# Performance work log

Measured on AMD Instinct MI355X. Metric: run time of the kernel, lower is better.

The kernel has to match this reference:

```python
import jax, jax.numpy as jnp
import numpy as np

H = 256  # hidden size; gates are 4H=1024 in PyTorch order i,f,g,o


def _lstm_layer(xs, W_ih, W_hh, b):
    """xs: (T, B, in) time-major. Returns (ys (T,B,H), (h_T, c_T))."""
    B = xs.shape[1]
    h0 = jnp.zeros((B, H), xs.dtype)
    c0 = jnp.zeros((B, H), xs.dtype)

    def step(carry, x_t):
        h, c = carry
        g = x_t @ W_ih.T + h @ W_hh.T + b  # (B, 4H)
        i, f, gg, o = jnp.split(g, 4, axis=-1)
        c = jax.nn.sigmoid(f) * c + jax.nn.sigmoid(i) * jnp.tanh(gg)
        h = jax.nn.sigmoid(o) * jnp.tanh(c)
        return (h, c), h

    (hT, cT), ys = jax.lax.scan(step, (h0, c0), xs)
    return ys, (hT, cT)


def setup_inputs() -> dict:
    key = jax.random.key(0)
    ks = jax.random.split(key, 9)
    B, T, D = 16, 8192, 7
    s = 0.05  # keep activations in a sane range
    return {
        "x": jax.random.normal(ks[0], (B, T, D), jnp.float32),
        "W_ih0": jax.random.normal(ks[1], (4 * H, D), jnp.float32) * s,
        "W_hh0": jax.random.normal(ks[2], (4 * H, H), jnp.float32) * s,
        "b0": jax.random.normal(ks[3], (4 * H,), jnp.float32) * s,
        "W_ih1": jax.random.normal(ks[4], (4 * H, H), jnp.float32) * s,
        "W_hh1": jax.random.normal(ks[5], (4 * H, H), jnp.float32) * s,
        "b1": jax.random.normal(ks[6], (4 * H,), jnp.float32) * s,
        "W_head": jax.random.normal(ks[7], (D, H), jnp.float32) * s,
        "b_head": jax.random.normal(ks[8], (D,), jnp.float32) * s,
    }


def reference(x, W_ih0, W_hh0, b0, W_ih1, W_hh1, b1, W_head, b_head):
    xs = jnp.transpose(x, (1, 0, 2))            # (T, B, D) time-major
    y0, (h0, c0) = _lstm_layer(xs, W_ih0, W_hh0, b0)
    y1, (h1, c1) = _lstm_layer(y0, W_ih1, W_hh1, b1)
    out = y1 @ W_head.T + b_head                # (T, B, out_dim)
    out = jnp.transpose(out, (1, 0, 2))         # (B, T, out_dim)
    h_n = jnp.stack([h0, h1])                   # (layers, B, H)
    c_n = jnp.stack([c0, c1])
    return (out, h_n, c_n)
```

## Files before the change

### kernel.cpp

```cpp
#include <hip/hip_runtime.h>
#include <hip/hip_bf16.h>

#define TT 8192
#define BB 16
#define HH 256
#define GG 8
#define NKS0 9
#define NKS1 16
#define ROW0 320
#define ROW1 512

typedef unsigned short u16;
typedef unsigned int   u32;
typedef __attribute__((ext_vector_type(4))) float f32x4;
typedef __attribute__((ext_vector_type(8))) short bf16x8;

union U16X8 { uint4 u; bf16x8 s; };

static const size_t OFF_SLOT = 0;
static const size_t OFF_H0   = 1024;
static const size_t OFF_H1   = 33792;
static const size_t OFF_A0   = 50176;
static const size_t OFF_A1   = 640000;
static const size_t OFF_Y1   = 1688576;

__device__ __forceinline__ float blo(u32 u){ return __uint_as_float(u << 16); }
__device__ __forceinline__ float bhi(u32 u){ return __uint_as_float(u & 0xffff0000u); }
__device__ __forceinline__ float sigf(float x){ return 1.0f/(1.0f + __expf(-x)); }
__device__ __forceinline__ float tanhf_(float x){ return 1.0f - 2.0f/(__expf(2.0f*x) + 1.0f); }
__device__ __forceinline__ u16 f2bf(float v){
  union { __hip_bfloat16 b; u16 s; } u; u.b = __float2bfloat16(v); return u.s;
}

__global__ __launch_bounds__(256) void pack_frags(
    const float* __restrict__ Wih0, const float* __restrict__ Whh0,
    const float* __restrict__ Wih1, const float* __restrict__ Whh1,
    u16* __restrict__ a0, u16* __restrict__ a1) {
  int idx = blockIdx.x*256 + threadIdx.x;
  const int N0 = GG*4*2*NKS0*512;
  const int N1 = GG*4*2*NKS1*512;
  if (idx < N0) {
    int i = idx;
    int ii = i & 511; int lane = ii >> 3; int e = ii & 7;
    int f = i >> 9; int ks = f % NKS0; f /= NKS0;
    int rt = f & 1; f >>= 1; int wq = f & 3; int g = f >> 2;
    int row = wq*256 + g*32 + rt*16 + (lane & 15);
    int k = ks*32 + (lane >> 4)*8 + e;
    float v = 0.0f;
    if (k < 7)                   v = Wih0[row*7 + k];
    else if (k >= 32 && k < 288) v = Whh0[row*256 + (k - 32)];
    a0[i] = f2bf(v);
  } else if (idx < N0 + N1) {
    int i = idx - N0;
    int ii = i & 511; int lane = ii >> 3; int e = ii & 7;
    int f = i >> 9; int ks = f & 15; f >>= 4;
    int rt = f & 1; f >>= 1; int wq = f & 3; int g = f >> 2;
    int row = wq*256 + g*32 + rt*16 + (lane & 15);
    int k = ks*32 + (lane >> 4)*8 + e;
    float v = (k < 256) ? Wih1[row*256 + k] : Whh1[row*256 + (k - 256)];
    a1[i] = f2bf(v);
  }
}

__device__ __forceinline__ void gang_wait(u32* slots_, int i, int tid, int l, int* budget) {
  if (i > 0) {
    if (tid < 64) {
      bool done = false;
      while (!done) {
        u32 v = 0xFFFFFFFFu;
        if (l < 16)
          v = __hip_atomic_load(&slots_[l*16], __ATOMIC_RELAXED, __HIP_MEMORY_SCOPE_AGENT);
        done = (bool)__all((int)(v >= (u32)i));
        if (!done) { __builtin_amdgcn_s_sleep(1); if (--(*budget) <= 0) done = true; }
      }
      (void)__hip_atomic_load(&slots_[0], __ATOMIC_ACQUIRE, __HIP_MEMORY_SCOPE_AGENT);
    }
    __syncthreads();
  }
}

__device__ __forceinline__ void gang_arrive(u32* slots_, int gb, int i, int tid) {
  asm volatile("s_waitcnt vmcnt(0)" ::: "memory");
  __syncthreads();
  if (tid == 0)
    __hip_atomic_store(&slots_[gb*16], (u32)(i + 1),
                       __ATOMIC_RELAXED, __HIP_MEMORY_SCOPE_AGENT);
}

__global__ __launch_bounds__(256, 1) void gangs(
    const float* __restrict__ x,
    const u16* __restrict__ a0, const u16* __restrict__ a1,
    const float* __restrict__ b0, const float* __restrict__ b1,
    u32* __restrict__ h0c, u32* __restrict__ h1c,
    u32* __restrict__ slots_, u32* __restrict__ y1ws,
    float* __restrict__ dout) {
  const int gb = blockIdx.x, tid = threadIdx.x;
  const int l = tid & 63, wq = tid >> 6;
  const int bb_ = l & 15, cq = l >> 4;
  const int pb = tid >> 4, pu = tid & 15;
  const int sb = tid >> 4, kg = tid & 15;
  __shared__ __align__(16) u16 hlds[16*ROW1];
  __shared__ float pre[4][32][17];
  uint4* lds4 = (uint4*)hlds;
  int budget = 3000000;
  float cst[2] = {0.f, 0.f}, hl[2] = {0.f, 0.f};

  if (gb < GG) {
    const int g = gb;
    uint4 A[2][NKS0];
    #pragma unroll
    for (int rt = 0; rt < 2; ++rt)
      #pragma unroll
      for (int ks = 0; ks < NKS0; ++ks)
        A[rt][ks] = ((const uint4*)a0)[ (((g*4 + wq)*2 + rt)*NKS0 + ks)*64 + l ];
    float bias4[2][4];
    #pragma unroll
    for (int rt = 0; rt < 2; ++rt)
      #pragma unroll
      for (int i = 0; i < 4; ++i)
        bias4[rt][i] = b0[wq*256 + g*32 + rt*16 + cq*4 + i];
    const int xb = tid >> 3, xj = tid & 7;
    for (int z = tid; z < 16*ROW0/2; z += 256) ((u32*)hlds)[z] = 0;
    __syncthreads();

    for (int i = 0; i < TT + 2; ++i) {
      const int t = i;
      const bool act = (t < TT);
      float xv = 0.0f;
      if (act && tid < 128 && xj < 7)
        xv = x[(size_t)xb*(TT*7) + (size_t)t*7 + xj];

      gang_wait(slots_, i, tid, l, &budget);

      if (act) {
        {
          const uint4* hb = (const uint4*)(h0c + ((t + 3) & 3)*2048 + sb*128 + kg*8);
          uint4 h0v = hb[0], h1v = hb[1];
          lds4[sb*40 + ((4 + 2*kg + 0) ^ (sb & 7))] = h0v;
          lds4[sb*40 + ((4 + 2*kg + 1) ^ (sb & 7))] = h1v;
        }
        if (tid < 128 && xj < 7)
          hlds[xb*ROW0 + ((xb & 7)*8) + xj] = f2bf(xv);
        __syncthreads();

        f32x4 acc[2];
        #pragma unroll
        for (int rt = 0; rt < 2; ++rt)
          acc[rt] = (f32x4){bias4[rt][0], bias4[rt][1], bias4[rt][2], bias4[rt][3]};
        #pragma unroll
        for (int ks = 0; ks < NKS0; ++ks) {
          U16X8 bfr; bfr.u = lds4[bb_*40 + ((ks*4 + cq) ^ (bb_ & 7))];
          U16X8 afr0; afr0.u = A[0][ks];
          U16X8 afr1; afr1.u = A[1][ks];
          acc[0] = __builtin_amdgcn_mfma_f32_16x16x32_bf16(afr0.s, bfr.s, acc[0], 0, 0, 0);
          acc[1] = __builtin_amdgcn_mfma_f32_16x16x32_bf16(afr1.s, bfr.s, acc[1], 0, 0, 0);
        }
        #pragma unroll
        for (int rt = 0; rt < 2; ++rt)
          #pragma unroll
          for (int ii = 0; ii < 4; ++ii)
            pre[wq][rt*16 + cq*4 + ii][bb_] = acc[rt][ii];
        __syncthreads();

        u32 packed;
        {
          #pragma unroll
          for (int e = 0; e < 2; ++e) {
            int u = 2*pu + e;
            float pi = pre[0][u][pb], pf = pre[1][u][pb],
                  pg = pre[2][u][pb], po = pre[3][u][pb];
            cst[e] = sigf(pf)*cst[e] + sigf(pi)*tanhf_(pg);
            hl[e]  = sigf(po)*tanhf_(cst[e]);
          }
          packed = (u32)f2bf(hl[0]) | ((u32)f2bf(hl[1]) << 16);
        }
        __hip_atomic_store(&h0c[(t & 3)*2048 + pb*128 + g*16 + pu], packed,
                           __ATOMIC_RELAXED, __HIP_MEMORY_SCOPE_AGENT);
      }
      gang_arrive(slots_, gb, i, tid);
    }
    #pragma unroll
    for (int e = 0; e < 2; ++e) {
      dout[917504 + pb*256 + g*32 + 2*pu + e] = hl[e];
      dout[925696 + pb*256 + g*32 + 2*pu + e] = cst[e];
    }
  } else {
    const int g = gb - GG;
    uint4 A[2][NKS1];
    #pragma unroll
    for (int rt = 0; rt < 2; ++rt)
      #pragma unroll
      for (int ks = 0; ks < NKS1; ++ks)
        A[rt][ks] = ((const uint4*)a1)[ (((g*4 + wq)*2 + rt)*NKS1 + ks)*64 + l ];
    float bias4[2][4];
    #pragma unroll
    for (int rt = 0; rt < 2; ++rt)
      #pragma unroll
      for (int i = 0; i < 4; ++i)
        bias4[rt][i] = b1[wq*256 + g*32 + rt*16 + cq*4 + i];
    __syncthreads();

    for (int i = 0; i < TT + 2; ++i) {
      const int t1 = i - 2;
      const bool act = (t1 >= 0);
      uint4 py[4];
      if (act && kg < 8) {
        const uint4* yb = (const uint4*)(h0c + (t1 & 3)*2048 + sb*128 + kg*16);
        #pragma unroll
        for (int m = 0; m < 4; ++m) py[m] = yb[m];
      }

      gang_wait(slots_, i, tid, l, &budget);

      if (act) {
        if (kg < 8) {
          #pragma unroll
          for (int m = 0; m < 4; ++m)
            lds4[sb*64 + ((4*kg + m) ^ (sb & 7))] = py[m];
        } else {
          const uint4* hb = (const uint4*)(h1c + (t1 & 1)*2048 + sb*128 + (kg - 8)*16);
          #pragma unroll
          for (int m = 0; m < 4; ++m)
            lds4[sb*64 + ((4*kg + m) ^ (sb & 7))] = hb[m];
        }
        __syncthreads();

        f32x4 acc[2];
        #pragma unroll
        for (int rt = 0; rt < 2; ++rt)
          acc[rt] = (f32x4){bias4[rt][0], bias4[rt][1], bias4[rt][2], bias4[rt][3]};
        #pragma unroll
        for (int ks = 0; ks < NKS1; ++ks) {
          U16X8 bfr; bfr.u = lds4[bb_*64 + ((ks*4 + cq) ^ (bb_ & 7))];
          U16X8 afr0; afr0.u = A[0][ks];
          U16X8 afr1; afr1.u = A[1][ks];
          acc[0] = __builtin_amdgcn_mfma_f32_16x16x32_bf16(afr0.s, bfr.s, acc[0], 0, 0, 0);
          acc[1] = __builtin_amdgcn_mfma_f32_16x16x32_bf16(afr1.s, bfr.s, acc[1], 0, 0, 0);
        }
        #pragma unroll
        for (int rt = 0; rt < 2; ++rt)
          #pragma unroll
          for (int ii = 0; ii < 4; ++ii)
            pre[wq][rt*16 + cq*4 + ii][bb_] = acc[rt][ii];
        __syncthreads();

        u32 packed;
        {
          #pragma unroll
          for (int e = 0; e < 2; ++e) {
            int u = 2*pu + e;
            float pi = pre[0][u][pb], pf = pre[1][u][pb],
                  pg = pre[2][u][pb], po = pre[3][u][pb];
            cst[e] = sigf(pf)*cst[e] + sigf(pi)*tanhf_(pg);
            hl[e]  = sigf(po)*tanhf_(cst[e]);
          }
          packed = (u32)f2bf(hl[0]) | ((u32)f2bf(hl[1]) << 16);
        }
        __hip_atomic_store(&h1c[((t1 + 1) & 1)*2048 + pb*128 + g*16 + pu], packed,
                           __ATOMIC_RELAXED, __HIP_MEMORY_SCOPE_AGENT);
        y1ws[(size_t)t1*2048 + pb*128 + g*16 + pu] = packed;
      }
      gang_arrive(slots_, gb, i, tid);
    }
    #pragma unroll
    for (int e = 0; e < 2; ++e) {
      dout[917504 + 4096 + pb*256 + g*32 + 2*pu + e] = hl[e];
      dout[925696 + 4096 + pb*256 + g*32 + 2*pu + e] = cst[e];
    }
  }
}

__global__ __launch_bounds__(256) void head_kernel(
    const u16* __restrict__ y1, const float* __restrict__ Wh,
    const float* __restrict__ bh, float* __restrict__ out) {
  __shared__ float wt[256][8];
  const int tid = threadIdx.x;
  for (int idx = tid; idx < 2048; idx += 256) {
    int j = idx >> 3, o = idx & 7;
    wt[j][o] = (o < 7) ? Wh[o*256 + j] : 0.0f;
  }
  __syncthreads();
  const int gidx = blockIdx.x*256 + tid;
  const int t = gidx >> 4, b = gidx & 15;
  const uint4* row = (const uint4*)(y1 + (size_t)t*4096 + b*256);
  float4 a03 = {0,0,0,0}, a47 = {0,0,0,0};
  #pragma unroll 4
  for (int jj = 0; jj < 32; ++jj) {
    uint4 v = row[jj];
    u32 ws_[4] = {v.x, v.y, v.z, v.w};
    #pragma unroll
    for (int m = 0; m < 4; ++m) {
      int j = jj*8 + 2*m;
      float h0 = blo(ws_[m]), h1 = bhi(ws_[m]);
      float4 w00 = *(const float4*)&wt[j][0],   w01 = *(const float4*)&wt[j][4];
      float4 w10 = *(const float4*)&wt[j+1][0], w11 = *(const float4*)&wt[j+1][4];
      a03.x += h0*w00.x; a03.y += h0*w00.y; a03.z += h0*w00.z; a03.w += h0*w00.w;
      a47.x += h0*w01.x; a47.y += h0*w01.y; a47.z += h0*w01.z;
      a03.x += h1*w10.x; a03.y += h1*w10.y; a03.z += h1*w10.z; a03.w += h1*w10.w;
      a47.x += h1*w11.x; a47.y += h1*w11.y; a47.z += h1*w11.z;
    }
  }
  const size_t ob = ((size_t)b*TT + t)*7;
  out[ob+0] = a03.x + bh[0]; out[ob+1] = a03.y + bh[1];
  out[ob+2] = a03.z + bh[2]; out[ob+3] = a03.w + bh[3];
  out[ob+4] = a47.x + bh[4]; out[ob+5] = a47.y + bh[5];
  out[ob+6] = a47.z + bh[6];
}

extern "C" void kernel_launch(void* const* d_in, const int* in_sizes, int n_in,
                              void* d_out, int out_size, void* d_ws, size_t ws_size,
                              hipStream_t stream) {
  const float* x     = (const float*)d_in[0];
  const float* Wih0  = (const float*)d_in[1];
  const float* Whh0  = (const float*)d_in[2];
  const float* b0    = (const float*)d_in[3];
  const float* Wih1  = (const float*)d_in[4];
  const float* Whh1  = (const float*)d_in[5];
  const float* b1    = (const float*)d_in[6];
  const float* Whead = (const float*)d_in[7];
  const float* bhead = (const float*)d_in[8];
  char* ws = (char*)d_ws;
  u32* slots = (u32*)(ws + OFF_SLOT);
  u32* h0c   = (u32*)(ws + OFF_H0);
  u32* h1c   = (u32*)(ws + OFF_H1);
  u16* a0    = (u16*)(ws + OFF_A0);
  u16* a1    = (u16*)(ws + OFF_A1);
  u32* y1ws  = (u32*)(ws + OFF_Y1);
  float* out = (float*)d_out;

  hipMemsetAsync(ws, 0, OFF_A0, stream);

  pack_frags<<<3200, 256, 0, stream>>>(Wih0, Whh0, Wih1, Whh1, a0, a1);
  gangs<<<2*GG, 256, 0, stream>>>(x, a0, a1, b0, b1, h0c, h1c, slots, y1ws, out);
  head_kernel<<<(TT*BB)/256, 256, 0, stream>>>((const u16*)y1ws, Whead, bhead, out);
}
```

Measured before the change: 26.08 ms.

## Replace global gang barrier with per-producer dataflow flags and ring buffers

Drops the all-block barrier that ran every step. Each consumer thread now spins only on the slot of the producer block whose h slice it needs, so layer 0 and layer 1 advance on point-to-point dependencies and layer 1 can lag layer 0 by several steps through an 8-deep ring. The hidden-state layout is regrouped per producer block so each thread reads a contiguous chunk with 64-bit atomic loads, and layer 0 waits on layer 1 for ring backpressure. This decouples the two layers and removes the sleep/ballot barrier latency, but adds many more polling threads, relies on relaxed atomics with no explicit acquire, and needs a larger workspace.

Result: no change. 26.21 ms (+0.5%).

```diff
diff --git a/kernel.cpp b/kernel.cpp
--- a/kernel.cpp
+++ b/kernel.cpp
@@ -9,9 +9,12 @@
 #define NKS1 16
 #define ROW0 320
 #define ROW1 512
+#define RING0 8
+#define RING1 4
 
 typedef unsigned short u16;
 typedef unsigned int   u32;
+typedef unsigned long long u64;
 typedef __attribute__((ext_vector_type(4))) float f32x4;
 typedef __attribute__((ext_vector_type(8))) short bf16x8;
 
@@ -19,10 +22,10 @@
 
 static const size_t OFF_SLOT = 0;
 static const size_t OFF_H0   = 1024;
-static const size_t OFF_H1   = 33792;
-static const size_t OFF_A0   = 50176;
-static const size_t OFF_A1   = 640000;
-static const size_t OFF_Y1   = 1688576;
+static const size_t OFF_H1   = 66560;
+static const size_t OFF_A0   = 99328;
+static const size_t OFF_A1   = 689152;
+static const size_t OFF_Y1   = 1737728;
 
 __device__ __forceinline__ float blo(u32 u){ return __uint_as_float(u << 16); }
 __device__ __forceinline__ float bhi(u32 u){ return __uint_as_float(u & 0xffff0000u); }
@@ -30,6 +33,18 @@
 __device__ __forceinline__ float tanhf_(float x){ return 1.0f - 2.0f/(__expf(2.0f*x) + 1.0f); }
 __device__ __forceinline__ u16 f2bf(float v){
   union { __hip_bfloat16 b; u16 s; } u; u.b = __float2bfloat16(v); return u.s;
+}
+__device__ __forceinline__ u32 ld_slot(const u32* p) {
+  return __hip_atomic_load(p, __ATOMIC_RELAXED, __HIP_MEMORY_SCOPE_AGENT);
+}
+__device__ __forceinline__ u64 ld_d2(const u32* p) {
+  return __hip_atomic_load((const u64*)p, __ATOMIC_RELAXED, __HIP_MEMORY_SCOPE_AGENT);
+}
+__device__ __forceinline__ void st_d(u32* p, u32 v) {
+  __hip_atomic_store(p, v, __ATOMIC_RELAXED, __HIP_MEMORY_SCOPE_AGENT);
+}
+__device__ __forceinline__ uint4 mk4(u64 a, u64 b) {
+  return make_uint4((u32)a, (u32)(a >> 32), (u32)b, (u32)(b >> 32));
 }
 
 __global__ __launch_bounds__(256) void pack_frags(
@@ -62,29 +77,10 @@
   }
 }
 
-__device__ __forceinline__ void gang_wait(u32* slots_, int i, int tid, int l, int* budget) {
-  if (i > 0) {
-    if (tid < 64) {
-      bool done = false;
-      while (!done) {
-        u32 v = 0xFFFFFFFFu;
-        if (l < 16)
-          v = __hip_atomic_load(&slots_[l*16], __ATOMIC_RELAXED, __HIP_MEMORY_SCOPE_AGENT);
-        done = (bool)__all((int)(v >= (u32)i));
-        if (!done) { __builtin_amdgcn_s_sleep(1); if (--(*budget) <= 0) done = true; }
-      }
-      (void)__hip_atomic_load(&slots_[0], __ATOMIC_ACQUIRE, __HIP_MEMORY_SCOPE_AGENT);
-    }
-    __syncthreads();
-  }
-}
-
-__device__ __forceinline__ void gang_arrive(u32* slots_, int gb, int i, int tid) {
+__device__ __forceinline__ void arrive(u32* slots_, int idx, int r, int tid) {
   asm volatile("s_waitcnt vmcnt(0)" ::: "memory");
   __syncthreads();
-  if (tid == 0)
-    __hip_atomic_store(&slots_[gb*16], (u32)(i + 1),
-                       __ATOMIC_RELAXED, __HIP_MEMORY_SCOPE_AGENT);
+  if (tid == 0) st_d(&slots_[idx], (u32)(r + 1));
 }
 
 __global__ __launch_bounds__(256, 1) void gangs(
@@ -98,11 +94,10 @@
   const int l = tid & 63, wq = tid >> 6;
   const int bb_ = l & 15, cq = l >> 4;
   const int pb = tid >> 4, pu = tid & 15;
-  const int sb = tid >> 4, kg = tid & 15;
   __shared__ __align__(16) u16 hlds[16*ROW1];
   __shared__ float pre[4][32][17];
   uint4* lds4 = (uint4*)hlds;
-  int budget = 3000000;
+  int budget = 4000000;
   float cst[2] = {0.f, 0.f}, hl[2] = {0.f, 0.f};
 
   if (gb < GG) {
@@ -120,64 +115,64 @@
       for (int i = 0; i < 4; ++i)
         bias4[rt][i] = b0[wq*256 + g*32 + rt*16 + cq*4 + i];
     const int xb = tid >> 3, xj = tid & 7;
+    const int s = tid >> 5, j = tid & 31;
     for (int z = tid; z < 16*ROW0/2; z += 256) ((u32*)hlds)[z] = 0;
     __syncthreads();
 
-    for (int i = 0; i < TT + 2; ++i) {
-      const int t = i;
-      const bool act = (t < TT);
+    for (int r = 0; r < TT; ++r) {
       float xv = 0.0f;
-      if (act && tid < 128 && xj < 7)
-        xv = x[(size_t)xb*(TT*7) + (size_t)t*7 + xj];
-
-      gang_wait(slots_, i, tid, l, &budget);
-
-      if (act) {
-        {
-          const uint4* hb = (const uint4*)(h0c + ((t + 3) & 3)*2048 + sb*128 + kg*8);
-          uint4 h0v = hb[0], h1v = hb[1];
-          lds4[sb*40 + ((4 + 2*kg + 0) ^ (sb & 7))] = h0v;
-          lds4[sb*40 + ((4 + 2*kg + 1) ^ (sb & 7))] = h1v;
-        }
-        if (tid < 128 && xj < 7)
-          hlds[xb*ROW0 + ((xb & 7)*8) + xj] = f2bf(xv);
-        __syncthreads();
-
-        f32x4 acc[2];
+      if (tid < 128 && xj < 7)
+        xv = x[(size_t)xb*(TT*7) + (size_t)r*7 + xj];
+
+      if (r > 0) {
+        while (ld_slot(&slots_[s]) < (u32)r) { if (--budget <= 0) break; }
+      }
+      const u32* bp = h0c + ((r + RING0 - 1) & (RING0-1))*2048
+                          + s*256 + (j >> 1)*16 + (j & 1)*8;
+      u64 d0 = ld_d2(bp), d1 = ld_d2(bp + 2), d2 = ld_d2(bp + 4), d3 = ld_d2(bp + 6);
+      if (r >= RING0 && tid < 8) {
+        while (ld_slot(&slots_[8 + tid]) < (u32)(r - (RING0-1))) { if (--budget <= 0) break; }
+      }
+      if (tid < 128 && xj < 7)
+        hlds[xb*ROW0 + ((xb & 7)*8) + xj] = f2bf(xv);
+      {
+        const int b = j >> 1, m = s*4 + (j & 1)*2;
+        lds4[b*40 + ((4 + m)     ^ (b & 7))] = mk4(d0, d1);
+        lds4[b*40 + ((4 + m + 1) ^ (b & 7))] = mk4(d2, d3);
+      }
+      __syncthreads();
+
+      f32x4 acc[2];
+      #pragma unroll
+      for (int rt = 0; rt < 2; ++rt)
+        acc[rt] = (f32x4){bias4[rt][0], bias4[rt][1], bias4[rt][2], bias4[rt][3]};
+      #pragma unroll
+      for (int ks = 0; ks < NKS0; ++ks) {
+        U16X8 bfr; bfr.u = lds4[bb_*40 + ((ks*4 + cq) ^ (bb_ & 7))];
+        U16X8 afr0; afr0.u = A[0][ks];
+        U16X8 afr1; afr1.u = A[1][ks];
+        acc[0] = __builtin_amdgcn_mfma_f32_16x16x32_bf16(afr0.s, bfr.s, acc[0], 0, 0, 0);
+        acc[1] = __builtin_amdgcn_mfma_f32_16x16x32_bf16(afr1.s, bfr.s, acc[1], 0, 0, 0);
+      }
+      #pragma unroll
+      for (int rt = 0; rt < 2; ++rt)
         #pragma unroll
-        for (int rt = 0; rt < 2; ++rt)
-          acc[rt] = (f32x4){bias4[rt][0], bias4[rt][1], bias4[rt][2], bias4[rt][3]};
-        #pragma unroll
-        for (int ks = 0; ks < NKS0; ++ks) {
-          U16X8 bfr; bfr.u = lds4[bb_*40 + ((ks*4 + cq) ^ (bb_ & 7))];
-          U16X8 afr0; afr0.u = A[0][ks];
-          U16X8 afr1; afr1.u = A[1][ks];
-          acc[0] = __builtin_amdgcn_mfma_f32_16x16x32_bf16(afr0.s, bfr.s, acc[0], 0, 0, 0);
-          acc[1] = __builtin_amdgcn_mfma_f32_16x16x32_bf16(afr1.s, bfr.s, acc[1], 0, 0, 0);
-        }
-        #pragma unroll
-        for (int rt = 0; rt < 2; ++rt)
-          #pragma unroll
-          for (int ii = 0; ii < 4; ++ii)
-            pre[wq][rt*16 + cq*4 + ii][bb_] = acc[rt][ii];
-        __syncthreads();
-
-        u32 packed;
-        {
-          #pragma unroll
-          for (int e = 0; e < 2; ++e) {
-            int u = 2*pu + e;
-            float pi = pre[0][u][pb], pf = pre[1][u][pb],
-                  pg = pre[2][u][pb], po = pre[3][u][pb];
-            cst[e] = sigf(pf)*cst[e] + sigf(pi)*tanhf_(pg);
-            hl[e]  = sigf(po)*tanhf_(cst[e]);
-          }
-          packed = (u32)f2bf(hl[0]) | ((u32)f2bf(hl[1]) << 16);
-        }
-        __hip_atomic_store(&h0c[(t & 3)*2048 + pb*128 + g*16 + pu], packed,
-                           __ATOMIC_RELAXED, __HIP_MEMORY_SCOPE_AGENT);
-      }
-      gang_arrive(slots_, gb, i, tid);
+        for (int ii = 0; ii < 4; ++ii)
+          pre[wq][rt*16 + cq*4 + ii][bb_] = acc[rt][ii];
+      __syncthreads();
+
+      u32 packed;
+      #pragma unroll
+      for (int e = 0; e < 2; ++e) {
+        int u = 2*pu + e;
+        float pi = pre[0][u][pb], pf = pre[1][u][pb],
+              pg = pre[2][u][pb], po = pre[3][u][pb];
+        cst[e] = sigf(pf)*cst[e] + sigf(pi)*tanhf_(pg);
+        hl[e]  = sigf(po)*tanhf_(cst[e]);
+      }
+      packed = (u32)f2bf(hl[0]) | ((u32)f2bf(hl[1]) << 16);
+      st_d(&h0c[(r & (RING0-1))*2048 + g*256 + pb*16 + pu], packed);
+      arrive(slots_, g, r, tid);
     }
     #pragma unroll
     for (int e = 0; e < 2; ++e) {
@@ -198,69 +193,62 @@
       #pragma unroll
       for (int i = 0; i < 4; ++i)
         bias4[rt][i] = b1[wq*256 + g*32 + rt*16 + cq*4 + i];
+    const int hsel = (tid < 128) ? 0 : 1;
+    const int tt = tid & 127, s = tt >> 4, j = tt & 15;
     __syncthreads();
 
-    for (int i = 0; i < TT + 2; ++i) {
-      const int t1 = i - 2;
-      const bool act = (t1 >= 0);
-      uint4 py[4];
-      if (act && kg < 8) {
-        const uint4* yb = (const uint4*)(h0c + (t1 & 3)*2048 + sb*128 + kg*16);
+    for (int t1 = 0; t1 < TT; ++t1) {
+      if (hsel == 0) {
+        while (ld_slot(&slots_[s]) < (u32)(t1 + 1)) { if (--budget <= 0) break; }
+      } else if (t1 > 0) {
+        while (ld_slot(&slots_[8 + s]) < (u32)t1) { if (--budget <= 0) break; }
+      }
+      const u32* bp = (hsel == 0)
+        ? h0c + (t1 & (RING0-1))*2048 + s*256 + j*16
+        : h1c + ((t1 + RING1 - 1) & (RING1-1))*2048 + s*256 + j*16;
+      u64 d[8];
+      #pragma unroll
+      for (int m = 0; m < 8; ++m) d[m] = ld_d2(bp + 2*m);
+      {
+        const int cb = hsel*32 + s*4;
         #pragma unroll
-        for (int m = 0; m < 4; ++m) py[m] = yb[m];
-      }
-
-      gang_wait(slots_, i, tid, l, &budget);
-
-      if (act) {
-        if (kg < 8) {
-          #pragma unroll
-          for (int m = 0; m < 4; ++m)
-            lds4[sb*64 + ((4*kg + m) ^ (sb & 7))] = py[m];
-        } else {
-          const uint4* hb = (const uint4*)(h1c + (t1 & 1)*2048 + sb*128 + (kg - 8)*16);
-          #pragma unroll
-          for (int m = 0; m < 4; ++m)
-            lds4[sb*64 + ((4*kg + m) ^ (sb & 7))] = hb[m];
-        }
-        __syncthreads();
-
-        f32x4 acc[2];
+        for (int c = 0; c < 4; ++c)
+          lds4[j*64 + ((cb + c) ^ (j & 7))] = mk4(d[2*c], d[2*c+1]);
+      }
+      __syncthreads();
+
+      f32x4 acc[2];
+      #pragma unroll
+      for (int rt = 0; rt < 2; ++rt)
+        acc[rt] = (f32x4){bias4[rt][0], bias4[rt][1], bias4[rt][2], bias4[rt][3]};
+      #pragma unroll
+      for (int ks = 0; ks < NKS1; ++ks) {
+        U16X8 bfr; bfr.u = lds4[bb_*64 + ((ks*4 + cq) ^ (bb_ & 7))];
+        U16X8 afr0; afr0.u = A[0][ks];
+        U16X8 afr1; afr1.u = A[1][ks];
+        acc[0] = __builtin_amdgcn_mfma_f32_16x16x32_bf16(afr0.s, bfr.s, acc[0], 0, 0, 0);
+        acc[1] = __builtin_amdgcn_mfma_f32_16x16x32_bf16(afr1.s, bfr.s, acc[1], 0, 0, 0);
+      }
+      #pragma unroll
+      for (int rt = 0; rt < 2; ++rt)
         #pragma unroll
-        for (int rt = 0; rt < 2; ++rt)
-          acc[rt] = (f32x4){bias4[rt][0], bias4[rt][1], bias4[rt][2], bias4[rt][3]};
-        #pragma unroll
-        for (int ks = 0; ks < NKS1; ++ks) {
-          U16X8 bfr; bfr.u = lds4[bb_*64 + ((ks*4 + cq) ^ (bb_ & 7))];
-          U16X8 afr0; afr0.u = A[0][ks];
-          U16X8 afr1; afr1.u = A[1][ks];
-          acc[0] = __builtin_amdgcn_mfma_f32_16x16x32_bf16(afr0.s, bfr.s, acc[0], 0, 0, 0);
-          acc[1] = __builtin_amdgcn_mfma_f32_16x16x32_bf16(afr1.s, bfr.s, acc[1], 0, 0, 0);
-        }
-        #pragma unroll
-        for (int rt = 0; rt < 2; ++rt)
-          #pragma unroll
-          for (int ii = 0; ii < 4; ++ii)
-            pre[wq][rt*16 + cq*4 + ii][bb_] = acc[rt][ii];
-        __syncthreads();
-
-        u32 packed;
-        {
-          #pragma unroll
-          for (int e = 0; e < 2; ++e) {
-            int u = 2*pu + e;
-            float pi = pre[0][u][pb], pf = pre[1][u][pb],
-                  pg = pre[2][u][pb], po = pre[3][u][pb];
-            cst[e] = sigf(pf)*cst[e] + sigf(pi)*tanhf_(pg);
-            hl[e]  = sigf(po)*tanhf_(cst[e]);
-          }
-          packed = (u32)f2bf(hl[0]) | ((u32)f2bf(hl[1]) << 16);
-        }
-        __hip_atomic_store(&h1c[((t1 + 1) & 1)*2048 + pb*128 + g*16 + pu], packed,
-                           __ATOMIC_RELAXED, __HIP_MEMORY_SCOPE_AGENT);
-        y1ws[(size_t)t1*2048 + pb*128 + g*16 + pu] = packed;
-      }
-      gang_arrive(slots_, gb, i, tid);
+        for (int ii = 0; ii < 4; ++ii)
+          pre[wq][rt*16 + cq*4 + ii][bb_] = acc[rt][ii];
+      __syncthreads();
+
+      u32 packed;
+      #pragma unroll
+      for (int e = 0; e < 2; ++e) {
+        int u = 2*pu + e;
+        float pi = pre[0][u][pb], pf = pre[1][u][pb],
+              pg = pre[2][u][pb], po = pre[3][u][pb];
+        cst[e] = sigf(pf)*cst[e] + sigf(pi)*tanhf_(pg);
+        hl[e]  = sigf(po)*tanhf_(cst[e]);
+      }
+      packed = (u32)f2bf(hl[0]) | ((u32)f2bf(hl[1]) << 16);
+      st_d(&h1c[(t1 & (RING1-1))*2048 + g*256 + pb*16 + pu], packed);
+      y1ws[(size_t)t1*2048 + pb*128 + g*16 + pu] = packed;
+      arrive(slots_, 8 + g, t1, tid);
     }
     #pragma unroll
     for (int e = 0; e < 2; ++e) {
```
